# Kernel tuning notes

Hardware: AMD Instinct MI355X
Metric: run time of the kernel (lower is better)

Reference implementation:

```python
import jax, jax.numpy as jnp
import numpy as np
import math

B, DSET, DOUT, DH, H, L, M, C = 32, 512, 16, 1024, 16, 6, 127, 8
S = M + 1            # sos + maximum_components targets
DHEAD = DH // H
DIN = DSET + 1 + 2 * DOUT  # embedding input dim = 545
DTOK = 1 + 2 * DOUT        # per-step token dim = 33


def _pos_encoding(max_len, d):
    pos = np.arange(max_len, dtype=np.float32)[:, None]
    div = np.exp(np.arange(0, d, 2, dtype=np.float32) * (-math.log(10000.0) / d))
    pe = np.zeros((max_len, d), dtype=np.float32)
    pe[:, 0::2] = np.sin(pos * div)
    pe[:, 1::2] = np.cos(pos * div)
    return jnp.asarray(pe[None])  # [1, max_len, d]


def setup_inputs() -> dict:
    key = jax.random.key(0)
    ks = iter(jax.random.split(key, 64))
    def n(shape, s=0.02):
        return jax.random.normal(next(ks), shape, jnp.float32) * s
    return {
        "input": jax.random.normal(next(ks), (B, DSET), jnp.float32),
        "targets": jax.random.normal(next(ks), (B, M, DTOK), jnp.float32),
        "W_emb": n((DH, DIN)), "b_emb": jnp.zeros((DH,), jnp.float32),
        "sos": jax.random.normal(next(ks), (1, 1, DTOK), jnp.float32),
        "Wqkv": n((L, 3 * DH, DH)), "bqkv": jnp.zeros((L, 3 * DH), jnp.float32),
        "Wo": n((L, DH, DH)), "bo": jnp.zeros((L, DH), jnp.float32),
        "W1": n((L, DH, DH)), "b1": jnp.zeros((L, DH), jnp.float32),
        "W2": n((L, DH, DH)), "b2": jnp.zeros((L, DH), jnp.float32),
        "g1": jnp.ones((L, DH), jnp.float32), "be1": jnp.zeros((L, DH), jnp.float32),
        "g2": jnp.ones((L, DH), jnp.float32), "be2": jnp.zeros((L, DH), jnp.float32),
        "Wm": n((1, DH)), "bm": jnp.zeros((1,), jnp.float32),
        "Wpi_m": n((C, DH)), "bpi_m": jnp.zeros((C,), jnp.float32),
        "Wmu_m": n((C * DOUT, DH)), "bmu_m": jnp.zeros((C * DOUT,), jnp.float32),
        "Wsg_m": n((C * DOUT, DH)), "bsg_m": jnp.zeros((C * DOUT,), jnp.float32),
        "Wpi_v": n((C, DH)), "bpi_v": jnp.zeros((C,), jnp.float32),
        "Wmu_v": n((C * DOUT, DH)), "bmu_v": jnp.zeros((C * DOUT,), jnp.float32),
        "Wsg_v": n((C * DOUT, DH)), "bsg_v": jnp.zeros((C * DOUT,), jnp.float32),
    }


def _ln(x, g, b, eps=1e-5):
    m = x.mean(-1, keepdims=True)
    v = ((x - m) ** 2).mean(-1, keepdims=True)
    return (x - m) / jnp.sqrt(v + eps) * g + b


def _layer(x, Wqkv, bqkv, Wo, bo, W1, b1, W2, b2, g1, be1, g2, be2, causal):
    # PyTorch TransformerEncoderLayer (post-norm, relu, dropout=0)
    qkv = x @ Wqkv.T + bqkv                       # [B,S,3*DH]
    q, k, v = jnp.split(qkv, 3, axis=-1)
    q = q.reshape(B, -1, H, DHEAD)
    k = k.reshape(B, -1, H, DHEAD)
    v = v.reshape(B, -1, H, DHEAD)
    sc = jnp.einsum('bqhd,bkhd->bhqk', q, k) / math.sqrt(DHEAD)
    sc = jnp.where(causal, sc, -1e30)
    a = jax.nn.softmax(sc, -1)
    o = jnp.einsum('bhqk,bkhd->bqhd', a, v).reshape(B, -1, DH)
    x = _ln(x + o @ Wo.T + bo, g1, be1)
    ff = jax.nn.relu(x @ W1.T + b1) @ W2.T + b2
    return _ln(x + ff, g2, be2)


def _mdn(h, Wpi, bpi, Wmu, bmu, Wsg, bsg):
    pi = jax.nn.softmax(h @ Wpi.T + bpi, -1)                      # [B,M,C]
    mu = (h @ Wmu.T + bmu).reshape(h.shape[:-1] + (C, DOUT))      # [B,M,C,DOUT]
    var = jnp.exp(h @ Wsg.T + bsg).reshape(h.shape[:-1] + (C, DOUT))
    return pi, mu, var


def reference(input, targets, W_emb, b_emb, sos, Wqkv, bqkv, Wo, bo, W1, b1, W2, b2,
              g1, be1, g2, be2, Wm, bm, Wpi_m, bpi_m, Wmu_m, bmu_m, Wsg_m, bsg_m,
              Wpi_v, bpi_v, Wmu_v, bmu_v, Wsg_v, bsg_v):
    pe = _pos_encoding(3 * M, DH)
    tokens = jnp.broadcast_to(sos, (B, 1, DTOK))
    cond = jnp.broadcast_to(input[:, None, :], (B, S, DSET))
    seq = jnp.concatenate([tokens, targets], axis=1)              # [B,S,DTOK]
    x = jnp.concatenate([cond, seq], axis=-1) @ W_emb.T + b_emb
    x = x + pe[:, :S, :]
    causal = jnp.tril(jnp.ones((S, S), bool))[None, None]
    for i in range(L):
        x = _layer(x, Wqkv[i], bqkv[i], Wo[i], bo[i], W1[i], b1[i], W2[i], b2[i],
                   g1[i], be1[i], g2[i], be2[i], causal)
    h = x[:, :-1, :]                                              # [B,M,DH]
    masks = h @ Wm.T + bm                                         # [B,M,1]
    pi_m, mu_m, var_m = _mdn(h, Wpi_m, bpi_m, Wmu_m, bmu_m, Wsg_m, bsg_m)
    pi_v, mu_v, var_v = _mdn(h, Wpi_v, bpi_v, Wmu_v, bmu_v, Wsg_v, bsg_v)
    return (pi_m, mu_m, var_m, pi_v, mu_v, var_v, masks)
```

## Files before the change

kernel.cpp:

```cpp
#include <hip/hip_runtime.h>
#include <hip/hip_bf16.h>

typedef __hip_bfloat16 bf16;
typedef __attribute__((ext_vector_type(8))) short bfrag8;
typedef __attribute__((ext_vector_type(4))) float facc4;
typedef __attribute__((ext_vector_type(4))) unsigned short us4;
typedef __attribute__((ext_vector_type(8))) unsigned short us8;
typedef __attribute__((ext_vector_type(4))) float f32x4;

#define AS1C const __attribute__((address_space(1))) void
#define AS3  __attribute__((address_space(3))) void

__device__ __forceinline__ void gload_lds16(const void* src, void* dst) {
    __builtin_amdgcn_global_load_lds((AS1C*)src, (AS3*)dst, 16, 0, 0);
}

__device__ __forceinline__ unsigned short f2bf(float f) {
    unsigned u = __float_as_uint(f);
    unsigned r = u + 0x7FFFu + ((u >> 16) & 1u);
    return (unsigned short)(r >> 16);
}
__device__ __forceinline__ float bf2f(unsigned short u) {
    return __uint_as_float((unsigned)u << 16);
}

__global__ void prep_cvt_kernel(const float* __restrict__ input, const float* __restrict__ targets,
                                const float* __restrict__ sos, const float* __restrict__ W_emb,
                                const float* __restrict__ Wm, const float* __restrict__ Wpi_m,
                                const float* __restrict__ Wmu_m, const float* __restrict__ Wsg_m,
                                const float* __restrict__ Wpi_v, const float* __restrict__ Wmu_v,
                                const float* __restrict__ Wsg_v,
                                const float* __restrict__ bm, const float* __restrict__ bpi_m,
                                const float* __restrict__ bmu_m, const float* __restrict__ bsg_m,
                                const float* __restrict__ bpi_v, const float* __restrict__ bmu_v,
                                const float* __restrict__ bsg_v,
                                const float* __restrict__ Wqkv, const float* __restrict__ Wo,
                                const float* __restrict__ W1, const float* __restrict__ W2,
                                float* __restrict__ pe, bf16* __restrict__ xin,
                                bf16* __restrict__ wemb, bf16* __restrict__ whead,
                                float* __restrict__ bhead,
                                bf16* __restrict__ wqb, bf16* __restrict__ wob,
                                bf16* __restrict__ w1b, bf16* __restrict__ w2b) {
    int bid = blockIdx.x;
    int t = threadIdx.x;
    if (bid < 4608) {
        int l = bid / 768;
        int s = bid - l * 768;
        const float* src; bf16* dst;
        if (s < 384)      { src = Wqkv + (size_t)l * 3145728; dst = wqb + (size_t)l * 3145728; }
        else if (s < 512) { src = Wo + (size_t)l * 1048576; dst = wob + (size_t)l * 1048576; s -= 384; }
        else if (s < 640) { src = W1 + (size_t)l * 1048576; dst = w1b + (size_t)l * 1048576; s -= 512; }
        else              { src = W2 + (size_t)l * 1048576; dst = w2b + (size_t)l * 1048576; s -= 640; }
        size_t pbase = (size_t)s * 1024 + t;
#pragma unroll
        for (int it = 0; it < 4; ++it) {
            size_t o = (pbase + it * 256) * 8;
            const f32x4* p = (const f32x4*)(src + o);
            f32x4 v1 = __builtin_nontemporal_load(p);
            f32x4 v2 = __builtin_nontemporal_load(p + 1);
            us8 w8;
            w8[0] = f2bf(v1.x); w8[1] = f2bf(v1.y); w8[2] = f2bf(v1.z); w8[3] = f2bf(v1.w);
            w8[4] = f2bf(v2.x); w8[5] = f2bf(v2.y); w8[6] = f2bf(v2.z); w8[7] = f2bf(v2.w);
            *(us8*)(dst + o) = w8;
        }
    } else if (bid < 4736) {
        int s = bid - 4608;
        float4 v;
#pragma unroll
        for (int j = 0; j < 4; ++j) {
            int c = t * 4 + j;
            int i = c >> 1;
            float div = expf(-9.210340371976184f * (float)(2 * i) * (1.f / 1024.f));
            float a = (float)s * div;
            v[j] = (c & 1) ? cosf(a) : sinf(a);
        }
        *(float4*)(pe + (size_t)s * 1024 + t * 4) = v;
    } else if (bid < 5888) {
        int chunk = (bid - 4736) * 256 + t;
        int row = chunk / 72;
        int cc = chunk - row * 72;
        int b = row >> 7, s = row & 127;
        us8 w8;
        if (cc < 64) {
            const float* p = input + (size_t)b * 512 + cc * 8;
            float4 v1 = *(const float4*)p;
            float4 v2 = *(const float4*)(p + 4);
            w8[0] = f2bf(v1.x); w8[1] = f2bf(v1.y); w8[2] = f2bf(v1.z); w8[3] = f2bf(v1.w);
            w8[4] = f2bf(v2.x); w8[5] = f2bf(v2.y); w8[6] = f2bf(v2.z); w8[7] = f2bf(v2.w);
        } else {
#pragma unroll
            for (int j = 0; j < 8; ++j) {
                int col = cc * 8 + j;
                float v = 0.f;
                if (col < 545) {
                    int jj = col - 512;
                    v = (s == 0) ? sos[jj] : targets[((size_t)b * 127 + (s - 1)) * 33 + jj];
                }
                w8[j] = f2bf(v);
            }
        }
        *(us8*)(xin + (size_t)row * 576 + cc * 8) = w8;
    } else if (bid < 6176) {
        int chunk = (bid - 5888) * 256 + t;
        int row = chunk / 72;
        int cc = chunk - row * 72;
        us8 w8;
#pragma unroll
        for (int j = 0; j < 8; ++j) {
            int col = cc * 8 + j;
            w8[j] = f2bf(col < 545 ? W_emb[(size_t)row * 545 + col] : 0.f);
        }
        *(us8*)(wemb + (size_t)row * 576 + cc * 8) = w8;
    } else if (bid < 6496) {
        int chunk = (bid - 6176) * 256 + t;
        int r = chunk >> 7;
        int cc = chunk & 127;
        const float* wsrc = nullptr; int off = 0;
        if (r == 0)        { wsrc = Wm;    off = 0; }
        else if (r < 9)    { wsrc = Wpi_m; off = r - 1; }
        else if (r < 137)  { wsrc = Wmu_m; off = r - 9; }
        else if (r < 265)  { wsrc = Wsg_m; off = r - 137; }
        else if (r < 273)  { wsrc = Wpi_v; off = r - 265; }
        else if (r < 401)  { wsrc = Wmu_v; off = r - 273; }
        else if (r < 529)  { wsrc = Wsg_v; off = r - 401; }
        us8 w8;
        if (wsrc) {
            const float* p = wsrc + (size_t)off * 1024 + cc * 8;
            float4 v1 = *(const float4*)p;
            float4 v2 = *(const float4*)(p + 4);
            w8[0] = f2bf(v1.x); w8[1] = f2bf(v1.y); w8[2] = f2bf(v1.z); w8[3] = f2bf(v1.w);
            w8[4] = f2bf(v2.x); w8[5] = f2bf(v2.y); w8[6] = f2bf(v2.z); w8[7] = f2bf(v2.w);
        } else {
#pragma unroll
            for (int j = 0; j < 8; ++j) w8[j] = 0;
        }
        *(us8*)(whead + (size_t)r * 1024 + cc * 8) = w8;
    } else {
        if (t < 529) {
            const float* bsrc; int off;
            if (t == 0)       { bsrc = bm;    off = 0; }
            else if (t < 9)   { bsrc = bpi_m; off = t - 1; }
            else if (t < 137) { bsrc = bmu_m; off = t - 9; }
            else if (t < 265) { bsrc = bsg_m; off = t - 137; }
            else if (t < 273) { bsrc = bpi_v; off = t - 265; }
            else if (t < 401) { bsrc = bmu_v; off = t - 273; }
            else              { bsrc = bsg_v; off = t - 401; }
            bhead[t] = bsrc[off];
        }
    }
}

template<int EPI, int CFG>
__global__ __launch_bounds__(CFG ? 512 : 256, CFG ? 2 : 4) void gemm_bt(
    const bf16* __restrict__ A, const bf16* __restrict__ Bw,
    float* __restrict__ Cf, bf16* __restrict__ Cb,
    const float* __restrict__ bias, const float* __restrict__ pe,
    int M, int N, int K, int lda, int ldb, int ldc, long long Az, long long Cz)
{
    constexpr int NT  = CFG ? 512 : 256;
    constexpr int NB  = CFG ? 2 : 1;
    constexpr int MI  = CFG ? 2 : 4;
    constexpr int BK  = (CFG == 2) ? 128 : 64;
    constexpr int RB  = BK * 2;
    constexpr int CPR = BK / 8;
    constexpr int NCH = (128 * CPR) / NT;
    constexpr int KS  = BK / 32;
    __shared__ __align__(16) bf16 sA[NB][128 * BK];
    __shared__ __align__(16) bf16 sB[NB][128 * BK];
    const int t = threadIdx.x;
    const int w = t >> 6, la = t & 63;
    const int wm = CFG ? (w >> 1) * 32 : (w >> 1) * 64;
    const int wn = (w & 1) * 64;
    const int m0 = blockIdx.y * 128, n0 = blockIdx.x * 128;
    const int z = blockIdx.z;
    A += (long long)z * Az;

    facc4 zero4 = {0.f, 0.f, 0.f, 0.f};
    facc4 acc[MI][4];
#pragma unroll
    for (int mi = 0; mi < MI; ++mi)
#pragma unroll
        for (int ni = 0; ni < 4; ++ni) acc[mi][ni] = zero4;

    auto stage = [&](int buf, int kt) {
#pragma unroll
        for (int i = 0; i < NCH; ++i) {
            int c = i * NT + t;
            int r = c / CPR;
            int cc = c - r * CPR;
            int bc = (cc * 16) ^ ((r & 7) << 4);
            gload_lds16(A + (size_t)(m0 + r) * lda + kt + (bc >> 1),
                        (char*)sA[buf] + (size_t)c * 16);
            gload_lds16(Bw + (size_t)(n0 + r) * ldb + kt + (bc >> 1),
                        (char*)sB[buf] + (size_t)c * 16);
        }
    };
    auto compute = [&](int buf) {
#pragma unroll
        for (int ks = 0; ks < KS; ++ks) {
            bfrag8 af[MI], bfv[4];
            const int koffb = (ks * 32 + (la >> 4) * 8) * 2;
#pragma unroll
            for (int i = 0; i < MI; ++i) {
                int rowa = wm + i * 16 + (la & 15);
                af[i] = *(const bfrag8*)((const char*)sA[buf] + rowa * RB + (koffb ^ ((rowa & 7) << 4)));
            }
#pragma unroll
            for (int i = 0; i < 4; ++i) {
                int rowb = wn + i * 16 + (la & 15);
                bfv[i] = *(const bfrag8*)((const char*)sB[buf] + rowb * RB + (koffb ^ ((rowb & 7) << 4)));
            }
#pragma unroll
            for (int mi = 0; mi < MI; ++mi)
#pragma unroll
                for (int ni = 0; ni < 4; ++ni)
                    acc[mi][ni] = __builtin_amdgcn_mfma_f32_16x16x32_bf16(bfv[ni], af[mi], acc[mi][ni], 0, 0, 0);
        }
    };

    const int nk = K / BK;
    if constexpr (CFG) {
        stage(0, 0);
        __syncthreads();
        int cur = 0;
        for (int kt = 0; kt < nk; ++kt) {
            if (kt + 1 < nk) stage(cur ^ 1, (kt + 1) * BK);
            compute(cur);
            __syncthreads();
            cur ^= 1;
        }
    } else {
        for (int kt = 0; kt < nk; ++kt) {
            stage(0, kt * BK);
            __syncthreads();
            compute(0);
            __syncthreads();
        }
    }
#pragma unroll
    for (int mi = 0; mi < MI; ++mi) {
        int row = m0 + wm + mi * 16 + (la & 15);
#pragma unroll
        for (int ni = 0; ni < 4; ++ni) {
            int colb = n0 + wn + ni * 16 + (la >> 4) * 4;
            if constexpr (EPI == 3) {
                if (row >= M) continue;
#pragma unroll
                for (int j = 0; j < 4; ++j) {
                    int col = colb + j;
                    if (col < N)
                        Cf[(size_t)z * Cz + (size_t)row * ldc + col] = acc[mi][ni][j] + bias[col];
                }
            } else {
                float4 bv = *(const float4*)(bias + colb);
                facc4 v = acc[mi][ni];
                v[0] += bv.x; v[1] += bv.y; v[2] += bv.z; v[3] += bv.w;
                size_t cidx = (size_t)row * ldc + colb;
                if constexpr (EPI == 0) {
                    us4 o; o.x = f2bf(v[0]); o.y = f2bf(v[1]); o.z = f2bf(v[2]); o.w = f2bf(v[3]);
                    *(us4*)(Cb + cidx) = o;
                } else if constexpr (EPI == 1) {
                    us4 o;
                    o.x = f2bf(v[0] > 0.f ? v[0] : 0.f); o.y = f2bf(v[1] > 0.f ? v[1] : 0.f);
                    o.z = f2bf(v[2] > 0.f ? v[2] : 0.f); o.w = f2bf(v[3] > 0.f ? v[3] : 0.f);
                    *(us4*)(Cb + cidx) = o;
                } else {
                    float4 p = *(const float4*)(pe + (size_t)(row & 127) * 1024 + colb);
                    us4 o;
                    o.x = f2bf(v[0] + p.x); o.y = f2bf(v[1] + p.y);
                    o.z = f2bf(v[2] + p.z); o.w = f2bf(v[3] + p.w);
                    *(us4*)(Cb + cidx) = o;
                }
            }
        }
    }
}

__global__ __launch_bounds__(256) void attn_fused(const bf16* __restrict__ qkv, bf16* __restrict__ obf)
{
    __shared__ __align__(16) char lds[65536];
    char* sQ  = lds;
    char* sK  = lds + 16384;
    char* sS  = lds + 32768;
    char* sVT = lds;
    float* redm = (float*)(lds + 16384);
    float* reds = (float*)(lds + 16384 + 1024);

    const int t = threadIdx.x, w = t >> 6, la = t & 63;
    const int b = blockIdx.x >> 4, h = blockIdx.x & 15;
    const size_t base = (size_t)b * 128 * 3072 + (size_t)h * 64;

#pragma unroll
    for (int i = 0; i < 4; ++i) {
        int c = i * 256 + w * 64 + la;
        int r = c >> 3;
        int bc = ((c & 7) * 16) ^ ((r & 7) << 4);
        gload_lds16(qkv + base + (size_t)r * 3072 + (bc >> 1),
                    sQ + (size_t)(i * 256 + w * 64) * 16);
        gload_lds16(qkv + base + 1024 + (size_t)r * 3072 + (bc >> 1),
                    sK + (size_t)(i * 256 + w * 64) * 16);
    }
    __syncthreads();

    const int wm = (w >> 1) * 64, wn = (w & 1) * 64;
    facc4 zero4 = {0.f, 0.f, 0.f, 0.f};
    facc4 acc[4][4];
#pragma unroll
    for (int mi = 0; mi < 4; ++mi)
#pragma unroll
        for (int ni = 0; ni < 4; ++ni) acc[mi][ni] = zero4;
#pragma unroll
    for (int ks = 0; ks < 2; ++ks) {
        bfrag8 af[4], bfv[4];
        const int koffb = (ks * 32 + (la >> 4) * 8) * 2;
#pragma unroll
        for (int i = 0; i < 4; ++i) {
            int rowa = wm + i * 16 + (la & 15);
            af[i] = *(const bfrag8*)(sQ + rowa * 128 + (koffb ^ ((rowa & 7) << 4)));
            int rowb = wn + i * 16 + (la & 15);
            bfv[i] = *(const bfrag8*)(sK + rowb * 128 + (koffb ^ ((rowb & 7) << 4)));
        }
#pragma unroll
        for (int mi = 0; mi < 4; ++mi)
#pragma unroll
            for (int ni = 0; ni < 4; ++ni)
                acc[mi][ni] = __builtin_amdgcn_mfma_f32_16x16x32_bf16(bfv[ni], af[mi], acc[mi][ni], 0, 0, 0);
    }
    __syncthreads();

#pragma unroll
    for (int i = 0; i < 4; ++i) {
        int c = i * 256 + t;
        int r = c >> 3;
        int d0 = (c & 7) * 8;
        bfrag8 vv = *(const bfrag8*)(qkv + base + 2048 + (size_t)r * 3072 + d0);
#pragma unroll
        for (int j = 0; j < 8; ++j) {
            int d = d0 + j;
            *(short*)(sVT + d * 256 + ((2 * r) ^ ((d & 7) << 4))) = vv[j];
        }
    }

    const int colh = (w & 1) * 128;
    float tmpm[4], tmps[4];
#pragma unroll
    for (int mi = 0; mi < 4; ++mi) {
        int q = wm + mi * 16 + (la & 15);
        float mx = -1e30f;
#pragma unroll
        for (int ni = 0; ni < 4; ++ni) {
            int kb = wn + ni * 16 + (la >> 4) * 4;
#pragma unroll
            for (int j = 0; j < 4; ++j) {
                float s = acc[mi][ni][j] * 0.125f;
                acc[mi][ni][j] = s;
                if (kb + j <= q) mx = fmaxf(mx, s);
            }
        }
        mx = fmaxf(mx, __shfl_xor(mx, 16));
        mx = fmaxf(mx, __shfl_xor(mx, 32));
        float sm = 0.f;
#pragma unroll
        for (int ni = 0; ni < 4; ++ni) {
            int kb = wn + ni * 16 + (la >> 4) * 4;
#pragma unroll
            for (int j = 0; j < 4; ++j) {
                float e = (kb + j <= q) ? __expf(acc[mi][ni][j] - mx) : 0.f;
                acc[mi][ni][j] = e;
                sm += e;
            }
        }
        sm += __shfl_xor(sm, 16);
        sm += __shfl_xor(sm, 32);
        tmpm[mi] = mx; tmps[mi] = sm;
    }
    if ((la >> 4) == 0) {
#pragma unroll
        for (int mi = 0; mi < 4; ++mi) {
            redm[colh + wm + mi * 16 + la] = tmpm[mi];
            reds[colh + wm + mi * 16 + la] = tmps[mi];
        }
    }
    __syncthreads();
#pragma unroll
    for (int mi = 0; mi < 4; ++mi) {
        int q = wm + mi * 16 + (la & 15);
        float m0 = redm[q], m1 = redm[128 + q];
        float M = fmaxf(m0, m1);
        float tot = reds[q] * __expf(m0 - M) + reds[128 + q] * __expf(m1 - M);
        float sc = __expf(tmpm[mi] - M) / tot;
#pragma unroll
        for (int ni = 0; ni < 4; ++ni) {
            int kb = wn + ni * 16 + (la >> 4) * 4;
            us4 sv;
            sv.x = f2bf(acc[mi][ni][0] * sc); sv.y = f2bf(acc[mi][ni][1] * sc);
            sv.z = f2bf(acc[mi][ni][2] * sc); sv.w = f2bf(acc[mi][ni][3] * sc);
            *(us4*)(sS + q * 256 + ((2 * kb) ^ ((q & 7) << 4))) = sv;
        }
    }
    __syncthreads();

    const int wm2 = (w >> 1) * 64, wn2 = (w & 1) * 32;
    facc4 a2[4][2];
#pragma unroll
    for (int mi = 0; mi < 4; ++mi) { a2[mi][0] = zero4; a2[mi][1] = zero4; }
#pragma unroll
    for (int ks = 0; ks < 4; ++ks) {
        bfrag8 pa[4], vb[2];
        const int koffb = (ks * 32 + (la >> 4) * 8) * 2;
#pragma unroll
        for (int mi = 0; mi < 4; ++mi) {
            int rowa = wm2 + mi * 16 + (la & 15);
            pa[mi] = *(const bfrag8*)(sS + rowa * 256 + (koffb ^ ((rowa & 7) << 4)));
        }
#pragma unroll
        for (int ni = 0; ni < 2; ++ni) {
            int rowb = wn2 + ni * 16 + (la & 15);
            vb[ni] = *(const bfrag8*)(sVT + rowb * 256 + (koffb ^ ((rowb & 7) << 4)));
        }
#pragma unroll
        for (int mi = 0; mi < 4; ++mi)
#pragma unroll
            for (int ni = 0; ni < 2; ++ni)
                a2[mi][ni] = __builtin_amdgcn_mfma_f32_16x16x32_bf16(vb[ni], pa[mi], a2[mi][ni], 0, 0, 0);
    }
#pragma unroll
    for (int mi = 0; mi < 4; ++mi) {
        int s = wm2 + mi * 16 + (la & 15);
#pragma unroll
        for (int ni = 0; ni < 2; ++ni) {
            int db = wn2 + ni * 16 + (la >> 4) * 4;
            us4 ov;
            ov.x = f2bf(a2[mi][ni][0]); ov.y = f2bf(a2[mi][ni][1]);
            ov.z = f2bf(a2[mi][ni][2]); ov.w = f2bf(a2[mi][ni][3]);
            *(us4*)(obf + ((size_t)(b * 128 + s)) * 1024 + h * 64 + db) = ov;
        }
    }
}

__global__ __launch_bounds__(256) void ln_res_kernel(const bf16* __restrict__ go,
                                                     const bf16* __restrict__ res,
                                                     const float* __restrict__ g, const float* __restrict__ be,
                                                     bf16* __restrict__ xb_out)
{
    const int t = threadIdx.x;
    const int row = blockIdx.x * 2 + (t >> 7);
    const int ct = t & 127;
    size_t o = (size_t)row * 1024 + ct * 8;
    us8 gv8 = *(const us8*)(go + o);
    us8 rv8 = *(const us8*)(res + o);
    float v[8];
    float s = 0.f, q = 0.f;
#pragma unroll
    for (int j = 0; j < 8; ++j) {
        v[j] = bf2f(rv8[j]) + bf2f(gv8[j]);
        s += v[j];
        q += v[j] * v[j];
    }
#pragma unroll
    for (int off = 32; off; off >>= 1) {
        s += __shfl_xor(s, off);
        q += __shfl_xor(q, off);
    }
    __shared__ float ssum[4], sqs[4];
    if ((t & 63) == 0) { ssum[t >> 6] = s; sqs[t >> 6] = q; }
    __syncthreads();
    int rb = (t >> 7) * 2;
    s = ssum[rb] + ssum[rb + 1];
    q = sqs[rb] + sqs[rb + 1];
    float mean = s * (1.f / 1024.f);
    float var = q * (1.f / 1024.f) - mean * mean;
    float rstd = rsqrtf(var + 1e-5f);
    float4 g1v = *(const float4*)(g + ct * 8);
    float4 g2v = *(const float4*)(g + ct * 8 + 4);
    float4 b1v = *(const float4*)(be + ct * 8);
    float4 b2v = *(const float4*)(be + ct * 8 + 4);
    float ga[8] = {g1v.x, g1v.y, g1v.z, g1v.w, g2v.x, g2v.y, g2v.z, g2v.w};
    float ba[8] = {b1v.x, b1v.y, b1v.z, b1v.w, b2v.x, b2v.y, b2v.z, b2v.w};
    us8 ob;
#pragma unroll
    for (int j = 0; j < 8; ++j)
        ob[j] = f2bf((v[j] - mean) * rstd * ga[j] + ba[j]);
    *(us8*)(xb_out + o) = ob;
}

__global__ void finalize_kernel(const float* __restrict__ hout, float* __restrict__ out) {
    const size_t O_PI_M = 0, O_MU_M = 32512, O_VAR_M = 552704, O_PI_V = 1072896,
                 O_MU_V = 1105408, O_VAR_V = 1625600, O_MASK = 2145792;
    int rm = blockIdx.x;
    const float* hrow = hout + (size_t)rm * 529;
    int t = threadIdx.x;
    if (t < 128) {
        out[O_MU_M  + (size_t)rm * 128 + t] = hrow[9 + t];
        out[O_VAR_M + (size_t)rm * 128 + t] = expf(hrow[137 + t]);
        out[O_MU_V  + (size_t)rm * 128 + t] = hrow[273 + t];
        out[O_VAR_V + (size_t)rm * 128 + t] = expf(hrow[401 + t]);
    } else if (t == 128) {
        out[O_MASK + rm] = hrow[0];
    } else if (t == 129 || t == 130) {
        int boff = (t == 129) ? 1 : 265;
        size_t oo = ((t == 129) ? O_PI_M : O_PI_V) + (size_t)rm * 8;
        float v[8], mx = -1e30f;
#pragma unroll
        for (int j = 0; j < 8; ++j) { v[j] = hrow[boff + j]; mx = fmaxf(mx, v[j]); }
        float sm = 0.f;
#pragma unroll
        for (int j = 0; j < 8; ++j) { v[j] = expf(v[j] - mx); sm += v[j]; }
        float inv = 1.f / sm;
#pragma unroll
        for (int j = 0; j < 8; ++j) out[oo + j] = v[j] * inv;
    }
}

extern "C" void kernel_launch(void* const* d_in, const int* in_sizes, int n_in,
                              void* d_out, int out_size, void* d_ws, size_t ws_size,
                              hipStream_t stream) {
    (void)in_sizes; (void)n_in; (void)out_size; (void)ws_size;
    const float* input   = (const float*)d_in[0];
    const float* targets = (const float*)d_in[1];
    const float* W_emb   = (const float*)d_in[2];
    const float* b_emb   = (const float*)d_in[3];
    const float* sos     = (const float*)d_in[4];
    const float* Wqkv    = (const float*)d_in[5];
    const float* bqkv    = (const float*)d_in[6];
    const float* Wo      = (const float*)d_in[7];
    const float* bo      = (const float*)d_in[8];
    const float* W1      = (const float*)d_in[9];
    const float* b1      = (const float*)d_in[10];
    const float* W2      = (const float*)d_in[11];
    const float* b2      = (const float*)d_in[12];
    const float* g1      = (const float*)d_in[13];
    const float* be1     = (const float*)d_in[14];
    const float* g2      = (const float*)d_in[15];
    const float* be2     = (const float*)d_in[16];
    const float* Wm      = (const float*)d_in[17];
    const float* bm      = (const float*)d_in[18];
    const float* Wpi_m   = (const float*)d_in[19];
    const float* bpi_m   = (const float*)d_in[20];
    const float* Wmu_m   = (const float*)d_in[21];
    const float* bmu_m   = (const float*)d_in[22];
    const float* Wsg_m   = (const float*)d_in[23];
    const float* bsg_m   = (const float*)d_in[24];
    const float* Wpi_v   = (const float*)d_in[25];
    const float* bpi_v   = (const float*)d_in[26];
    const float* Wmu_v   = (const float*)d_in[27];
    const float* bmu_v   = (const float*)d_in[28];
    const float* Wsg_v   = (const float*)d_in[29];
    const float* bsg_v   = (const float*)d_in[30];
    float* out = (float*)d_out;

    char* ws = (char*)d_ws;
    float* pe      = (float*)(ws + 0);
    bf16*  xin     = (bf16*)(ws + 524288);
    bf16*  wemb    = (bf16*)(ws + 5242880);
    bf16*  whead   = (bf16*)(ws + 6422528);
    float* bhead   = (float*)(ws + 7733248);
    bf16*  xb      = (bf16*)(ws + 24513024);
    bf16*  qkvb    = (bf16*)(ws + 32901632);
    bf16*  ob      = (bf16*)(ws + 58067456);
    bf16*  tmpb    = (bf16*)(ws + 66456064);
    bf16*  wqb_all = (bf16*)(ws + 83233280);
    bf16*  wob_all = (bf16*)(ws + 120982016);
    bf16*  w1b_all = (bf16*)(ws + 133564928);
    bf16*  w2b_all = (bf16*)(ws + 146147840);
    float* hout    = (float*)(ws + 158730752);

    prep_cvt_kernel<<<6497, 256, 0, stream>>>(input, targets, sos, W_emb,
                                              Wm, Wpi_m, Wmu_m, Wsg_m, Wpi_v, Wmu_v, Wsg_v,
                                              bm, bpi_m, bmu_m, bsg_m, bpi_v, bmu_v, bsg_v,
                                              Wqkv, Wo, W1, W2,
                                              pe, xin, wemb, whead, bhead,
                                              wqb_all, wob_all, w1b_all, w2b_all);
    gemm_bt<4, 1><<<dim3(8, 32, 1), 512, 0, stream>>>(xin, wemb, nullptr, xb, b_emb, pe,
                                                      4096, 1024, 576, 576, 576, 1024, 0, 0);
    for (int l = 0; l < 6; ++l) {
        const bf16* wqb = wqb_all + (size_t)l * 3145728;
        const bf16* wob = wob_all + (size_t)l * 1048576;
        const bf16* w1b = w1b_all + (size_t)l * 1048576;
        const bf16* w2b = w2b_all + (size_t)l * 1048576;
        gemm_bt<0, 0><<<dim3(24, 32, 1), 256, 0, stream>>>(xb, wqb, nullptr, qkvb, bqkv + l * 3072,
                                                           nullptr, 4096, 3072, 1024, 1024, 1024, 3072, 0, 0);
        attn_fused<<<512, 256, 0, stream>>>(qkvb, ob);
        gemm_bt<0, 2><<<dim3(8, 32, 1), 512, 0, stream>>>(ob, wob, nullptr, tmpb, bo + l * 1024,
                                                          nullptr, 4096, 1024, 1024, 1024, 1024, 1024, 0, 0);
        ln_res_kernel<<<2048, 256, 0, stream>>>(tmpb, xb, g1 + l * 1024, be1 + l * 1024, xb);
        gemm_bt<1, 2><<<dim3(8, 32, 1), 512, 0, stream>>>(xb, w1b, nullptr, ob, b1 + l * 1024,
                                                          nullptr, 4096, 1024, 1024, 1024, 1024, 1024, 0, 0);
        gemm_bt<0, 2><<<dim3(8, 32, 1), 512, 0, stream>>>(ob, w2b, nullptr, tmpb, b2 + l * 1024,
                                                          nullptr, 4096, 1024, 1024, 1024, 1024, 1024, 0, 0);
        ln_res_kernel<<<2048, 256, 0, stream>>>(tmpb, xb, g2 + l * 1024, be2 + l * 1024, xb);
    }
    gemm_bt<3, 2><<<dim3(5, 1, 32), 512, 0, stream>>>(xb, whead, hout, nullptr, bhead, nullptr,
                                                      127, 529, 1024, 1024, 1024, 529, 131072LL, 67183LL);
    finalize_kernel<<<4064, 256, 0, stream>>>(hout, out);
}
```

Measured before the change: 732.4 us.

## Swizzle GEMM block order across XCDs, load Q directly to registers, add setprio

The GEMM kernel remaps its flat block index so that consecutive blocks land on the same XCD chiplet, aiming to improve L2 reuse of shared A/B tiles. The attention kernel now loads Q fragments straight from global memory into registers instead of staging them through LDS, which removes one LDS round trip. It also raises wave priority around the two MFMA loops. The register-held Q fragments add register pressure, and the swizzle only applies when the grid size is a multiple of 8.

```diff
diff --git a/kernel.cpp b/kernel.cpp
--- a/kernel.cpp
+++ b/kernel.cpp
@@ -171,7 +171,13 @@
     const int w = t >> 6, la = t & 63;
     const int wm = CFG ? (w >> 1) * 32 : (w >> 1) * 64;
     const int wn = (w & 1) * 64;
-    const int m0 = blockIdx.y * 128, n0 = blockIdx.x * 128;
+    int nwgxy = gridDim.x * gridDim.y;
+    int flat = blockIdx.y * gridDim.x + blockIdx.x;
+    if ((nwgxy & 7) == 0) {
+        int cpx = nwgxy >> 3;
+        flat = (flat & 7) * cpx + (flat >> 3);
+    }
+    const int m0 = (flat / gridDim.x) * 128, n0 = (flat % gridDim.x) * 128;
     const int z = blockIdx.z;
     A += (long long)z * Az;
 
@@ -279,7 +285,6 @@
 __global__ __launch_bounds__(256) void attn_fused(const bf16* __restrict__ qkv, bf16* __restrict__ obf)
 {
     __shared__ __align__(16) char lds[65536];
-    char* sQ  = lds;
     char* sK  = lds + 16384;
     char* sS  = lds + 32768;
     char* sVT = lds;
@@ -290,33 +295,40 @@
     const int b = blockIdx.x >> 4, h = blockIdx.x & 15;
     const size_t base = (size_t)b * 128 * 3072 + (size_t)h * 64;
 
+    const int wm = (w >> 1) * 64, wn = (w & 1) * 64;
+
 #pragma unroll
     for (int i = 0; i < 4; ++i) {
         int c = i * 256 + w * 64 + la;
         int r = c >> 3;
         int bc = ((c & 7) * 16) ^ ((r & 7) << 4);
-        gload_lds16(qkv + base + (size_t)r * 3072 + (bc >> 1),
-                    sQ + (size_t)(i * 256 + w * 64) * 16);
         gload_lds16(qkv + base + 1024 + (size_t)r * 3072 + (bc >> 1),
                     sK + (size_t)(i * 256 + w * 64) * 16);
     }
+    bfrag8 qf[4][2];
+#pragma unroll
+    for (int mi = 0; mi < 4; ++mi)
+#pragma unroll
+        for (int ks = 0; ks < 2; ++ks) {
+            int rowa = wm + mi * 16 + (la & 15);
+            int k0 = ks * 32 + (la >> 4) * 8;
+            qf[mi][ks] = *(const bfrag8*)(qkv + base + (size_t)rowa * 3072 + k0);
+        }
     __syncthreads();
 
-    const int wm = (w >> 1) * 64, wn = (w & 1) * 64;
     facc4 zero4 = {0.f, 0.f, 0.f, 0.f};
     facc4 acc[4][4];
 #pragma unroll
     for (int mi = 0; mi < 4; ++mi)
 #pragma unroll
         for (int ni = 0; ni < 4; ++ni) acc[mi][ni] = zero4;
+    __builtin_amdgcn_s_setprio(1);
 #pragma unroll
     for (int ks = 0; ks < 2; ++ks) {
-        bfrag8 af[4], bfv[4];
+        bfrag8 bfv[4];
         const int koffb = (ks * 32 + (la >> 4) * 8) * 2;
 #pragma unroll
         for (int i = 0; i < 4; ++i) {
-            int rowa = wm + i * 16 + (la & 15);
-            af[i] = *(const bfrag8*)(sQ + rowa * 128 + (koffb ^ ((rowa & 7) << 4)));
             int rowb = wn + i * 16 + (la & 15);
             bfv[i] = *(const bfrag8*)(sK + rowb * 128 + (koffb ^ ((rowb & 7) << 4)));
         }
@@ -324,8 +336,9 @@
         for (int mi = 0; mi < 4; ++mi)
 #pragma unroll
             for (int ni = 0; ni < 4; ++ni)
-                acc[mi][ni] = __builtin_amdgcn_mfma_f32_16x16x32_bf16(bfv[ni], af[mi], acc[mi][ni], 0, 0, 0);
-    }
+                acc[mi][ni] = __builtin_amdgcn_mfma_f32_16x16x32_bf16(bfv[ni], qf[mi][ks], acc[mi][ni], 0, 0, 0);
+    }
+    __builtin_amdgcn_s_setprio(0);
     __syncthreads();
 
 #pragma unroll
@@ -404,6 +417,7 @@
     facc4 a2[4][2];
 #pragma unroll
     for (int mi = 0; mi < 4; ++mi) { a2[mi][0] = zero4; a2[mi][1] = zero4; }
+    __builtin_amdgcn_s_setprio(1);
 #pragma unroll
     for (int ks = 0; ks < 4; ++ks) {
         bfrag8 pa[4], vb[2];
@@ -424,6 +438,7 @@
             for (int ni = 0; ni < 2; ++ni)
                 a2[mi][ni] = __builtin_amdgcn_mfma_f32_16x16x32_bf16(vb[ni], pa[mi], a2[mi][ni], 0, 0, 0);
     }
+    __builtin_amdgcn_s_setprio(0);
 #pragma unroll
     for (int mi = 0; mi < 4; ++mi) {
         int s = wm2 + mi * 16 + (la & 15);
```

New measurement: 708.5 us, median of 2. -3.3%, faster.
